# Kernel optimization log

Hardware: AMD Instinct MI355X
Metric: run time of the kernel (lower is better)

The kernel has to match this reference:

```python
import math
import jax, jax.numpy as jnp
import numpy as np

HEADS = 8
SCALE_BASE = 512.0
GN_EPS = 1e-5


def _gammas(heads):
    # 1 - exp(linspace(log(1/32), log(1/512), heads))
    return 1.0 - np.exp(np.linspace(math.log(1.0 / 32.0), math.log(1.0 / 512.0), heads))


def _xpos(x, downscale):
    # x: (N, S, d), d even. Faithful to torchscale XPOS with scale_base=512.
    N, S, d = x.shape
    half = d // 2
    scale = (jnp.arange(0, d, 2, dtype=jnp.float32) + 0.4 * d) / (1.4 * d)        # (half,)
    pos = jnp.arange(S, dtype=jnp.float32)
    sc = scale[None, :] ** (pos / SCALE_BASE)[:, None]                             # (S, half)
    inv_freq = 1.0 / (10000.0 ** (jnp.arange(half, dtype=jnp.float32) / half))
    sinusoid = pos[:, None] * inv_freq[None, :]                                    # (S, half)
    sin, cos = jnp.sin(sinusoid), jnp.cos(sinusoid)
    if downscale:
        sc = 1.0 / sc
    # duplicate_interleave == repeat each column twice adjacently
    sin_s = jnp.repeat(sin * sc, 2, axis=-1)                                       # (S, d)
    cos_s = jnp.repeat(cos * sc, 2, axis=-1)
    x1, x2 = x[..., ::2], x[..., 1::2]
    rot = jnp.stack((-x2, x1), axis=-1).reshape(x.shape)                           # rotate_every_two
    return x * cos_s + rot * sin_s


def setup_inputs() -> dict:
    key = jax.random.key(0)
    ks = jax.random.split(key, 6)
    B, S, H = 2, 2048, 1024
    h = HEADS
    d = H // h
    X = jax.random.normal(ks[0], (B, S, H), dtype=jnp.float32)
    # per-head projections, torch init: randn(d, d) / d
    W_Q = jax.random.normal(ks[1], (h, d, d), dtype=jnp.float32) / d
    W_K = jax.random.normal(ks[2], (h, d, d), dtype=jnp.float32) / d
    W_V = jax.random.normal(ks[3], (h, d, d), dtype=jnp.float32) / d
    W_G = jax.random.normal(ks[4], (H, H), dtype=jnp.float32) / H
    W_O = jax.random.normal(ks[5], (H, H), dtype=jnp.float32) / H
    gn_weight = jnp.ones((H,), dtype=jnp.float32)
    gn_bias = jnp.zeros((H,), dtype=jnp.float32)
    return {"X": X, "W_Q": W_Q, "W_K": W_K, "W_V": W_V,
            "W_G": W_G, "W_O": W_O, "gn_weight": gn_weight, "gn_bias": gn_bias}


def reference(X, W_Q, W_K, W_V, W_G, W_O, gn_weight, gn_bias):
    B, S, H = X.shape
    h = HEADS
    d = H // h
    gammas = jnp.asarray(_gammas(h), dtype=X.dtype)                                # (h,)

    Xh = X.reshape(B, S, h, d)
    Q = jnp.einsum('bshd,hde->bhse', Xh, W_Q)                                      # (B,h,S,d)
    K = jnp.einsum('bshd,hde->bhse', Xh, W_K)
    V = jnp.einsum('bshd,hde->bhse', Xh, W_V)

    Q = _xpos(Q.reshape(B * h, S, d), downscale=False).reshape(B, h, S, d)
    K = _xpos(K.reshape(B * h, S, d), downscale=True).reshape(B, h, S, d)

    # decay mask D[h, n, m] = gamma_h^(n-m) for n >= m else 0 (NaN-safe)
    n = jnp.arange(S)
    diff = n[:, None] - n[None, :]                                                 # (S,S)
    causal = (diff >= 0)
    D = (gammas[:, None, None] ** jnp.where(causal, diff, 0).astype(X.dtype)) \
        * causal[None].astype(X.dtype)                                             # (h,S,S)

    att = jnp.einsum('bhsd,bhtd->bhst', Q, K) * D[None]                            # (B,h,S,S)
    Y = jnp.einsum('bhst,bhtd->bshd', att, V).reshape(B, S, H)

    # GroupNorm(heads, hidden) over flattened (B*S, H), biased variance
    Yg = Y.reshape(B * S, h, d)
    mu = Yg.mean(axis=-1, keepdims=True)
    var = Yg.var(axis=-1, keepdims=True)
    Yn = ((Yg - mu) / jnp.sqrt(var + GN_EPS)).reshape(B * S, H)
    Yn = (Yn * gn_weight + gn_bias).reshape(B, S, H)

    G = X @ W_G
    return (G * jax.nn.sigmoid(G) * Yn) @ W_O
```

## Files before the change

### kernel.cpp

```cpp
#include <hip/hip_runtime.h>
#include <math.h>

#define NB 2
#define SEQ 2048
#define HD 1024
#define NH 8
#define DH 128
#define HALF 64

typedef __bf16 bf16_t;
typedef __attribute__((ext_vector_type(8))) __bf16 bf16x8;
typedef __attribute__((ext_vector_type(4))) __bf16 bf16x4;
typedef __attribute__((ext_vector_type(4))) float f32x4;

typedef __attribute__((address_space(1))) void gvoid;
typedef __attribute__((address_space(3))) void lvoid;

__device__ __forceinline__ void gld16(const bf16_t* g, bf16_t* l) {
  __builtin_amdgcn_global_load_lds((gvoid*)g, (lvoid*)l, 16, 0, 0);
}

__device__ __forceinline__ float head_l2g(int hh) {
  double ga = log(1.0/32.0), gbb = log(1.0/512.0);
  float gamma = (float)(1.0 - exp(ga + (double)hh * (gbb - ga) / 7.0));
  return log2f(gamma);
}

__global__ __launch_bounds__(256) void k_tables(float* __restrict__ tabs) {
  int idx = blockIdx.x * 256 + threadIdx.x;
  if (idx >= SEQ * HALF) return;
  int s = idx >> 6, i = idx & 63;
  float dd = (float)DH;
  float scale = (2.0f * (float)i + 0.4f * dd) / (1.4f * dd);
  float sc = expf(logf(scale) * ((float)s / 512.0f));
  float inv_freq = expf(-logf(10000.0f) * ((float)i / (float)HALF));
  float ang = (float)s * inv_freq;
  float sn, cs;
  sincosf(ang, &sn, &cs);
  float rsc = 1.0f / sc;
  tabs[idx]               = sn * sc;
  tabs[SEQ*HALF + idx]    = cs * sc;
  tabs[2*SEQ*HALF + idx]  = sn * rsc;
  tabs[3*SEQ*HALF + idx]  = cs * rsc;
}

__global__ __launch_bounds__(256) void k_wsplit(
    const float* __restrict__ in, bf16_t* __restrict__ oh, int M, int N) {
  __shared__ float tile[64][65];
  int z = blockIdx.z;
  in += (size_t)z * M * N; oh += (size_t)z * M * N;
  int r0 = blockIdx.y * 64, c0 = blockIdx.x * 64;
  int t = threadIdx.x;
  for (int idx = t; idx < 1024; idx += 256) {
    int r = idx >> 4, c4 = (idx & 15) * 4;
    float4 v = *(const float4*)(in + (size_t)(r0 + r) * N + c0 + c4);
    *(float4*)&tile[r][c4] = v;
  }
  __syncthreads();
  for (int idx = t; idx < 1024; idx += 256) {
    int c = idx >> 4, r4 = (idx & 15) * 4;
    bf16x4 h;
    #pragma unroll
    for (int j = 0; j < 4; ++j)
      h[j] = (bf16_t)tile[r4 + j][c];
    *(bf16x4*)(oh + (size_t)(c0 + c) * M + r0 + r4) = h;
  }
}

__global__ __launch_bounds__(256, 2) void k_qkv(
    const float* __restrict__ X, const float* __restrict__ tabs,
    const bf16_t* __restrict__ Wqt, const bf16_t* __restrict__ Wkt,
    const bf16_t* __restrict__ Wvt,
    bf16_t* __restrict__ Qo, bf16_t* __restrict__ Ko,
    bf16_t* __restrict__ VTo, bf16_t* __restrict__ Xhg) {
  __shared__ bf16_t Wsh[128][128];
  int t = threadIdx.x;
  int lane = t & 63, w = t >> 6;
  int lr = lane & 15, lg = lane >> 4;
  int s0 = blockIdx.x * 64;
  int hh = blockIdx.y;
  int b  = blockIdx.z;
  size_t bh = (size_t)(b*NH + hh);

  bf16x8 xh[4];
  {
    const float* xp = X + ((size_t)(b*SEQ + s0 + 16*w + lr)) * HD + hh*DH + 8*lg;
    #pragma unroll
    for (int ks = 0; ks < 4; ++ks) {
      float4 u = *(const float4*)(xp + 32*ks);
      float4 v = *(const float4*)(xp + 32*ks + 4);
      float fv[8] = {u.x,u.y,u.z,u.w,v.x,v.y,v.z,v.w};
      #pragma unroll
      for (int j = 0; j < 8; ++j) xh[ks][j] = (bf16_t)fv[j];
    }
  }
  {
    bf16_t* xo = Xhg + ((size_t)(b*SEQ + s0 + 16*w + lr)) * HD + hh*DH + 8*lg;
    #pragma unroll
    for (int ks = 0; ks < 4; ++ks)
      *(bf16x8*)(xo + 32*ks) = xh[ks];
  }

  const bf16_t* Wp[3] = {Wqt, Wkt, Wvt};

  for (int which = 0; which < 3; ++which) {
    const bf16_t* wp = Wp[which] + (size_t)hh * (DH*DH);
    __syncthreads();
    for (int idx = t; idx < 2048; idx += 256) {
      int e = idx >> 4, kb = idx & 15;
      int kbs = kb ^ (e & 7);
      *(bf16x8*)&Wsh[e][kbs*8] = *(const bf16x8*)(wp + (size_t)e*DH + kb*8);
    }
    __syncthreads();
    f32x4 yacc[8];
    #pragma unroll
    for (int i = 0; i < 8; ++i) yacc[i] = (f32x4){0.f,0.f,0.f,0.f};
    #pragma unroll
    for (int sub = 0; sub < 8; ++sub) {
      int e = 16*sub + lr;
      #pragma unroll
      for (int ks = 0; ks < 4; ++ks) {
        int ch = (lg + 4*ks) ^ (lr & 7);
        bf16x8 bhv = *(const bf16x8*)&Wsh[e][ch*8];
        yacc[sub] = __builtin_amdgcn_mfma_f32_16x16x32_bf16(xh[ks], bhv, yacc[sub], 0, 0, 0);
      }
    }
    if (which < 2) {
      const float* st = tabs + (which ? 2*SEQ*HALF : 0);
      const float* ct = st + SEQ*HALF;
      bf16_t* Op = which ? Ko : Qo;
      #pragma unroll
      for (int sub = 0; sub < 8; ++sub) {
        int e = 16*sub + lr;
        int i = e >> 1;
        #pragma unroll
        for (int reg = 0; reg < 4; ++reg) {
          float v = yacc[sub][reg];
          float p = __shfl_xor(v, 1);
          int srow = s0 + 16*w + 4*lg + reg;
          float sv = st[srow*HALF + i], cv = ct[srow*HALF + i];
          float o = v * cv + ((e & 1) ? p : -p) * sv;
          Op[(bh*SEQ + srow) * DH + e] = (bf16_t)o;
        }
      }
    } else {
      #pragma unroll
      for (int sub = 0; sub < 8; ++sub) {
        int e = 16*sub + lr;
        bf16x4 hv;
        #pragma unroll
        for (int reg = 0; reg < 4; ++reg)
          hv[reg] = (bf16_t)yacc[sub][reg];
        *(bf16x4*)(VTo + bh * (size_t)(DH*SEQ) + (size_t)e*SEQ + (s0 + 16*w + 4*lg)) = hv;
      }
    }
  }
}

__global__ __launch_bounds__(256, 1) void k_delta(
    const bf16_t* __restrict__ Kg, const bf16_t* __restrict__ VTg,
    bf16_t* __restrict__ DSt) {
  __shared__ bf16_t KT[128][128];
  __shared__ bf16_t Vd[128][128];
  int t = threadIdx.x;
  int lane = t & 63, w = t >> 6;
  int lr = lane & 15, lg = lane >> 4;
  int c = blockIdx.x, bh = blockIdx.y, hh = bh & 7;
  float l2g = head_l2g(hh);
  size_t kbase = (size_t)bh * SEQ * DH + (size_t)c * 128 * DH;
  size_t vtb   = (size_t)bh * DH * SEQ + (size_t)c * 128;

  for (int idx = t; idx < 2048; idx += 256) {
    int dc = idx >> 7, tau = idx & 127;
    bf16x8 h8 = *(const bf16x8*)(Kg + kbase + (size_t)tau*DH + dc*8);
    #pragma unroll
    for (int j = 0; j < 8; ++j) {
      int d = dc*8 + j;
      int col = (((tau>>3) ^ (d & 7)) << 3) | (tau & 7);
      KT[d][col] = h8[j];
    }
  }
  for (int idx = t; idx < 2048; idx += 256) {
    int dv = idx >> 4, tc = idx & 15;
    bf16x8 h8 = *(const bf16x8*)(VTg + vtb + (size_t)dv*SEQ + tc*8);
    bf16x8 oh;
    #pragma unroll
    for (int j = 0; j < 8; ++j) {
      int tau = tc*8 + j;
      oh[j] = (bf16_t)((float)h8[j] * exp2f(l2g * (float)(127 - tau)));
    }
    int cs = tc ^ (dv & 7);
    *(bf16x8*)&Vd[dv][cs*8] = oh;
  }
  __syncthreads();

  f32x4 acc[2][8];
  #pragma unroll
  for (int i = 0; i < 2; ++i)
    #pragma unroll
    for (int s = 0; s < 8; ++s) acc[i][s] = (f32x4){0.f,0.f,0.f,0.f};

  #pragma unroll
  for (int i = 0; i < 2; ++i) {
    int dv = 32*w + 16*i + lr;
    #pragma unroll
    for (int ks = 0; ks < 4; ++ks) {
      int ca = (lg + 4*ks) ^ (dv & 7);
      bf16x8 avh = *(const bf16x8*)&Vd[dv][ca*8];
      #pragma unroll
      for (int sub = 0; sub < 8; ++sub) {
        int dk = 16*sub + lr;
        int cb = (lg + 4*ks) ^ (dk & 7);
        bf16x8 bkh = *(const bf16x8*)&KT[dk][cb*8];
        acc[i][sub] = __builtin_amdgcn_mfma_f32_16x16x32_bf16(avh, bkh, acc[i][sub], 0, 0, 0);
      }
    }
  }
  size_t obase = ((size_t)bh * 16 + c) * 16384;
  #pragma unroll
  for (int i = 0; i < 2; ++i)
    #pragma unroll
    for (int sub = 0; sub < 8; ++sub)
      #pragma unroll
      for (int reg = 0; reg < 4; ++reg) {
        int dv = 32*w + 16*i + 4*lg + reg;
        int dk = 16*sub + lr;
        DSt[obase + (size_t)dv*128 + dk] = (bf16_t)acc[i][sub][reg];
      }
}

__global__ __launch_bounds__(256) void k_scan(bf16_t* __restrict__ DSt) {
  int t = threadIdx.x;
  int bh = blockIdx.y, hh = bh & 7;
  float l2g = head_l2g(hh);
  float g128 = exp2f(l2g * 128.0f);
  int dv = blockIdx.x * 16 + (t >> 4);
  int dk0 = (t & 15) * 8;
  size_t base = ((size_t)bh * 16) * 16384 + (size_t)dv*128 + dk0;
  float S[8] = {};
  for (int c = 0; c < 16; ++c) {
    size_t off = base + (size_t)c * 16384;
    bf16x8 dh = *(const bf16x8*)(DSt + off);
    bf16x8 sh;
    #pragma unroll
    for (int j = 0; j < 8; ++j) sh[j] = (bf16_t)S[j];
    *(bf16x8*)(DSt + off) = sh;
    #pragma unroll
    for (int j = 0; j < 8; ++j)
      S[j] = g128*S[j] + (float)dh[j];
  }
}

__global__ __launch_bounds__(512, 1) void k_ret(
    const bf16_t* __restrict__ Qg, const bf16_t* __restrict__ Kg,
    const bf16_t* __restrict__ VTg, const bf16_t* __restrict__ DSt,
    const float* __restrict__ gw, const float* __restrict__ gb,
    float* __restrict__ Yn) {
  __shared__ bf16_t Ksh[64][128];
  __shared__ bf16_t Vsh[128][64];
  __shared__ bf16_t Ph[128][64];
  int t = threadIdx.x;
  int lane = t & 63, w = t >> 6;
  int lr = lane & 15, lg = lane >> 4;
  int c = blockIdx.x, bh = blockIdx.y, hh = bh & 7;
  int s0 = c * 128;
  size_t base  = (size_t)bh * SEQ * DH;
  size_t vbase = (size_t)bh * DH * SEQ;
  float l2g = head_l2g(hh);
  float colf = exp2f(-l2g * (float)lr);
  float g16v[4];
  #pragma unroll
  for (int ts = 0; ts < 4; ++ts) g16v[ts] = exp2f(-l2g * (float)(16*ts));

  bf16x8 qh[4];
  {
    const bf16_t* qp = Qg + base + (size_t)(s0 + 16*w + lr) * DH + lg * 8;
    #pragma unroll
    for (int ks = 0; ks < 4; ++ks)
      qh[ks] = *(const bf16x8*)(qp + 32*ks);
  }
  f32x4 yacc[8];
  #pragma unroll
  for (int i = 0; i < 8; ++i) yacc[i] = (f32x4){0.f,0.f,0.f,0.f};

  for (int idx = t; idx < 1024; idx += 512) {
    int r = idx >> 4, kb = idx & 15;
    int kbs = kb ^ (r & 7);
    *(bf16x8*)&Ksh[r][kbs*8] = *(const bf16x8*)(Kg + base + (size_t)(s0 + r)*DH + kb*8);
  }
  for (int idx = t; idx < 1024; idx += 512) {
    int d = idx >> 3, cb = idx & 7;
    int cbs = cb ^ (d & 7);
    *(bf16x8*)&Vsh[d][cbs*8] = *(const bf16x8*)(VTg + vbase + (size_t)d*SEQ + s0 + cb*8);
  }

  {
    const bf16_t* sth = DSt + ((size_t)bh * 16 + c) * 16384;
    #pragma unroll
    for (int sub = 0; sub < 8; ++sub) {
      size_t ro = (size_t)(16*sub + lr) * 128 + 8*lg;
      #pragma unroll
      for (int ks = 0; ks < 4; ++ks) {
        bf16x8 bh_ = *(const bf16x8*)(sth + ro + 32*ks);
        yacc[sub] = __builtin_amdgcn_mfma_f32_16x16x32_bf16(qh[ks], bh_, yacc[sub], 0, 0, 0);
      }
    }
    float rowc[4];
    #pragma unroll
    for (int reg = 0; reg < 4; ++reg)
      rowc[reg] = exp2f(l2g * (float)(16*w + 4*lg + reg + 1));
    #pragma unroll
    for (int sub = 0; sub < 8; ++sub)
      #pragma unroll
      for (int reg = 0; reg < 4; ++reg)
        yacc[sub][reg] *= rowc[reg];
  }
  __syncthreads();

  for (int kt = 0; kt < 2; ++kt) {
    int t0 = kt * 64;
    if (kt == 1) {
      __syncthreads();
      for (int idx = t; idx < 1024; idx += 512) {
        int r = idx >> 4, kb = idx & 15;
        int kbs = kb ^ (r & 7);
        *(bf16x8*)&Ksh[r][kbs*8] = *(const bf16x8*)(Kg + base + (size_t)(s0 + 64 + r)*DH + kb*8);
      }
      for (int idx = t; idx < 1024; idx += 512) {
        int d = idx >> 3, cb = idx & 7;
        int cbs = cb ^ (d & 7);
        *(bf16x8*)&Vsh[d][cbs*8] = *(const bf16x8*)(VTg + vbase + (size_t)d*SEQ + s0 + 64 + cb*8);
      }
    }
    __syncthreads();
    if (!(kt == 1 && w < 4)) {
      float rowf[4];
      #pragma unroll
      for (int reg = 0; reg < 4; ++reg)
        rowf[reg] = exp2f(l2g * (float)(16*w + 4*lg + reg - t0));

      #pragma unroll
      for (int ts = 0; ts < 4; ++ts) {
        f32x4 sacc = (f32x4){0.f,0.f,0.f,0.f};
        int trow = 16*ts + lr;
        #pragma unroll
        for (int ks = 0; ks < 4; ++ks) {
          int kbs = (4*ks + lg) ^ (trow & 7);
          bf16x8 kh8 = *(const bf16x8*)&Ksh[trow][kbs*8];
          sacc = __builtin_amdgcn_mfma_f32_16x16x32_bf16(qh[ks], kh8, sacc, 0, 0, 0);
        }
        float cf = colf * g16v[ts];
        #pragma unroll
        for (int reg = 0; reg < 4; ++reg) {
          int qloc = 4*lg + reg;
          int diff = (16*w + qloc) - (t0 + trow);
          float p = (diff >= 0) ? sacc[reg] * (rowf[reg] * cf) : 0.0f;
          int cb = (trow >> 3) ^ (qloc & 7);
          Ph[16*w + qloc][cb*8 + (trow & 7)] = (bf16_t)p;
        }
      }
      #pragma unroll
      for (int ks = 0; ks < 2; ++ks) {
        int prow = 16*w + lr;
        int pcb = (4*ks + lg) ^ (lr & 7);
        bf16x8 pah = *(const bf16x8*)&Ph[prow][pcb*8];
        #pragma unroll
        for (int sub = 0; sub < 8; ++sub) {
          int drow = 16*sub + lr;
          int vcb = (4*ks + lg) ^ (drow & 7);
          bf16x8 vh8 = *(const bf16x8*)&Vsh[drow][vcb*8];
          yacc[sub] = __builtin_amdgcn_mfma_f32_16x16x32_bf16(pah, vh8, yacc[sub], 0, 0, 0);
        }
      }
    }
  }

  float s1v[4] = {0.f,0.f,0.f,0.f}, s2v[4] = {0.f,0.f,0.f,0.f};
  #pragma unroll
  for (int sub = 0; sub < 8; ++sub)
    #pragma unroll
    for (int reg = 0; reg < 4; ++reg) {
      float v = yacc[sub][reg];
      s1v[reg] += v;
      s2v[reg] += v * v;
    }
  #pragma unroll
  for (int off = 8; off; off >>= 1)
    #pragma unroll
    for (int reg = 0; reg < 4; ++reg) {
      s1v[reg] += __shfl_xor(s1v[reg], off);
      s2v[reg] += __shfl_xor(s2v[reg], off);
    }
  float gwv[8], gbv[8];
  #pragma unroll
  for (int sub = 0; sub < 8; ++sub) {
    gwv[sub] = gw[hh*DH + 16*sub + lr];
    gbv[sub] = gb[hh*DH + 16*sub + lr];
  }
  int b = bh >> 3;
  #pragma unroll
  for (int reg = 0; reg < 4; ++reg) {
    float mean = s1v[reg] * (1.0f/128.0f);
    float var = s2v[reg] * (1.0f/128.0f) - mean*mean;
    float inv = rsqrtf(var + 1e-5f);
    int srow = s0 + 16*w + 4*lg + reg;
    float* op = Yn + (size_t)(b*SEQ + srow) * HD + hh*DH;
    #pragma unroll
    for (int sub = 0; sub < 8; ++sub)
      op[16*sub + lr] = (yacc[sub][reg] - mean) * inv * gwv[sub] + gbv[sub];
  }
}

__global__ __launch_bounds__(512, 1) void k_gemm(
    const bf16_t* __restrict__ Ag, const bf16_t* __restrict__ Bg,
    const float* __restrict__ E,
    bf16_t* __restrict__ Oh, float* __restrict__ Of, int mode) {
  __shared__ bf16_t SB[2][2][128][64];
  int t = threadIdx.x;
  int lane = t & 63, w = t >> 6;
  int lr = lane & 15, lg = lane >> 4;
  int wr = w >> 1, wc = w & 1;
  int bid = blockIdx.x;
  int swz = (bid & 7) * 32 + (bid >> 3);
  int n0 = (swz & 7) * 128, m0 = (swz >> 3) * 128;

  const bf16_t* srcs[2] = { Ag + (size_t)m0 * HD, Bg + (size_t)n0 * HD };

  f32x4 acc[2][4];
  #pragma unroll
  for (int i = 0; i < 2; ++i)
    #pragma unroll
    for (int j = 0; j < 4; ++j) acc[i][j] = (f32x4){0.f,0.f,0.f,0.f};

  int srow = lane >> 3, sch = lane & 7;

  #pragma unroll
  for (int bi = 0; bi < 2; ++bi)
    #pragma unroll
    for (int i = 0; i < 2; ++i) {
      int row = w*16 + i*8 + srow;
      int kc = (sch ^ (row & 7)) * 8;
      gld16(srcs[bi] + (size_t)row*HD + kc, &SB[bi][0][w*16 + i*8][0]);
    }
  __syncthreads();

  int buf = 0;
  for (int kt = 0; kt < 16; ++kt) {
    if (kt + 1 < 16) {
      int k0 = (kt + 1) * 64;
      #pragma unroll
      for (int bi = 0; bi < 2; ++bi)
        #pragma unroll
        for (int i = 0; i < 2; ++i) {
          int row = w*16 + i*8 + srow;
          int kc = (sch ^ (row & 7)) * 8;
          gld16(srcs[bi] + (size_t)row*HD + k0 + kc, &SB[bi][buf^1][w*16 + i*8][0]);
        }
    }
    #pragma unroll
    for (int ks = 0; ks < 2; ++ks) {
      bf16x8 a_[2], b_[4];
      #pragma unroll
      for (int mf = 0; mf < 2; ++mf) {
        int row = wr*32 + mf*16 + lr;
        int ch = (lg + 4*ks) ^ (row & 7);
        a_[mf] = *(const bf16x8*)&SB[0][buf][row][ch*8];
      }
      #pragma unroll
      for (int nf = 0; nf < 4; ++nf) {
        int row = wc*64 + nf*16 + lr;
        int ch = (lg + 4*ks) ^ (row & 7);
        b_[nf] = *(const bf16x8*)&SB[1][buf][row][ch*8];
      }
      #pragma unroll
      for (int mf = 0; mf < 2; ++mf)
        #pragma unroll
        for (int nf = 0; nf < 4; ++nf)
          acc[mf][nf] = __builtin_amdgcn_mfma_f32_16x16x32_bf16(a_[mf], b_[nf], acc[mf][nf], 0, 0, 0);
    }
    __syncthreads();
    buf ^= 1;
  }
  #pragma unroll
  for (int mf = 0; mf < 2; ++mf) {
    #pragma unroll
    for (int nf = 0; nf < 4; ++nf) {
      #pragma unroll
      for (int reg = 0; reg < 4; ++reg) {
        int m = m0 + wr*32 + mf*16 + 4*lg + reg;
        int n = n0 + wc*64 + nf*16 + lr;
        float g = acc[mf][nf][reg];
        size_t off = (size_t)m * HD + n;
        if (mode == 1) {
          float sg = 1.0f / (1.0f + expf(-g));
          Oh[off] = (bf16_t)(g * sg * E[off]);
        } else {
          Of[off] = g;
        }
      }
    }
  }
}

extern "C" void kernel_launch(void* const* d_in, const int* in_sizes, int n_in,
                              void* d_out, int out_size, void* d_ws, size_t ws_size,
                              hipStream_t stream) {
  const float* X  = (const float*)d_in[0];
  const float* Wq = (const float*)d_in[1];
  const float* Wk = (const float*)d_in[2];
  const float* Wv = (const float*)d_in[3];
  const float* Wg = (const float*)d_in[4];
  const float* Wo = (const float*)d_in[5];
  const float* gw = (const float*)d_in[6];
  const float* gb = (const float*)d_in[7];
  float* out = (float*)d_out;
  float* ws = (float*)d_ws;

  float* tabs = ws;
  bf16_t* Q   = (bf16_t*)(ws + 524288);
  bf16_t* K   = Q + 4194304;
  bf16_t* VT  = K + 4194304;
  float*  Yn  = (float*)(VT + 4194304);
  bf16_t* DSt = (bf16_t*)(Yn + 4194304);
  bf16_t* Wqt = DSt + 4194304;
  bf16_t* Wkt = Wqt + 131072;
  bf16_t* Wvt = Wkt + 131072;
  bf16_t* Wgt = Wvt + 131072;
  bf16_t* Wot = Wgt + 1048576;
  bf16_t* Xh  = Wot + 1048576;
  bf16_t* A2  = Q;

  k_tables<<<dim3(512), dim3(256), 0, stream>>>(tabs);
  k_wsplit<<<dim3(2, 2, 8), dim3(256), 0, stream>>>(Wq, Wqt, DH, DH);
  k_wsplit<<<dim3(2, 2, 8), dim3(256), 0, stream>>>(Wk, Wkt, DH, DH);
  k_wsplit<<<dim3(2, 2, 8), dim3(256), 0, stream>>>(Wv, Wvt, DH, DH);
  k_wsplit<<<dim3(16, 16, 1), dim3(256), 0, stream>>>(Wg, Wgt, HD, HD);
  k_wsplit<<<dim3(16, 16, 1), dim3(256), 0, stream>>>(Wo, Wot, HD, HD);
  k_qkv<<<dim3(32, 8, 2), dim3(256), 0, stream>>>(X, tabs, Wqt, Wkt, Wvt,
                                                  Q, K, VT, Xh);
  k_delta<<<dim3(16, 16), dim3(256), 0, stream>>>(K, VT, DSt);
  k_scan<<<dim3(8, 16), dim3(256), 0, stream>>>(DSt);
  k_ret<<<dim3(16, 16), dim3(512), 0, stream>>>(Q, K, VT, DSt, gw, gb, Yn);
  k_gemm<<<dim3(256), dim3(512), 0, stream>>>(Xh, Wgt, Yn, A2, nullptr, 1);
  k_gemm<<<dim3(256), dim3(512), 0, stream>>>(A2, Wot, nullptr, nullptr, out, 0);
}
```

Before: 116.4 us.

## Merge prep kernels, store normalized output in bf16, retile gated GEMMs

Merges the table-generation kernel and the five weight transpose/convert launches into a single prep kernel that dispatches on block index, removing five launches. The group-norm output Yn is now written in bf16 instead of fp32, which halves its write and re-read traffic in the gating GEMM. The two final GEMMs switch from 128x128 tiles with 512 threads to 64x128 tiles with 256 threads and two blocks per CU, doubling the grid and using an XCD-aware block mapping. Storing Yn in bf16 adds rounding error, and the smaller tiles reuse each loaded B tile across fewer rows.

```diff
diff --git a/kernel.cpp b/kernel.cpp
--- a/kernel.cpp
+++ b/kernel.cpp
@@ -26,30 +26,11 @@
   return log2f(gamma);
 }
 
-__global__ __launch_bounds__(256) void k_tables(float* __restrict__ tabs) {
-  int idx = blockIdx.x * 256 + threadIdx.x;
-  if (idx >= SEQ * HALF) return;
-  int s = idx >> 6, i = idx & 63;
-  float dd = (float)DH;
-  float scale = (2.0f * (float)i + 0.4f * dd) / (1.4f * dd);
-  float sc = expf(logf(scale) * ((float)s / 512.0f));
-  float inv_freq = expf(-logf(10000.0f) * ((float)i / (float)HALF));
-  float ang = (float)s * inv_freq;
-  float sn, cs;
-  sincosf(ang, &sn, &cs);
-  float rsc = 1.0f / sc;
-  tabs[idx]               = sn * sc;
-  tabs[SEQ*HALF + idx]    = cs * sc;
-  tabs[2*SEQ*HALF + idx]  = sn * rsc;
-  tabs[3*SEQ*HALF + idx]  = cs * rsc;
-}
-
-__global__ __launch_bounds__(256) void k_wsplit(
-    const float* __restrict__ in, bf16_t* __restrict__ oh, int M, int N) {
-  __shared__ float tile[64][65];
-  int z = blockIdx.z;
+__device__ void wsplit_body(const float* __restrict__ in, bf16_t* __restrict__ oh,
+                            int M, int N, int bx, int by, int z,
+                            float (*tile)[65]) {
   in += (size_t)z * M * N; oh += (size_t)z * M * N;
-  int r0 = blockIdx.y * 64, c0 = blockIdx.x * 64;
+  int r0 = by * 64, c0 = bx * 64;
   int t = threadIdx.x;
   for (int idx = t; idx < 1024; idx += 256) {
     int r = idx >> 4, c4 = (idx & 15) * 4;
@@ -64,6 +45,46 @@
     for (int j = 0; j < 4; ++j)
       h[j] = (bf16_t)tile[r4 + j][c];
     *(bf16x4*)(oh + (size_t)(c0 + c) * M + r0 + r4) = h;
+  }
+}
+
+__global__ __launch_bounds__(256) void k_prep(
+    const float* __restrict__ Wq, const float* __restrict__ Wk,
+    const float* __restrict__ Wv, const float* __restrict__ Wg,
+    const float* __restrict__ Wo,
+    float* __restrict__ tabs, bf16_t* __restrict__ Wqt,
+    bf16_t* __restrict__ Wkt, bf16_t* __restrict__ Wvt,
+    bf16_t* __restrict__ Wgt, bf16_t* __restrict__ Wot) {
+  __shared__ float tile[64][65];
+  int b = blockIdx.x;
+  if (b < 512) {
+    int idx = b * 256 + threadIdx.x;
+    int s = idx >> 6, i = idx & 63;
+    float dd = (float)DH;
+    float scale = (2.0f * (float)i + 0.4f * dd) / (1.4f * dd);
+    float sc = expf(logf(scale) * ((float)s / 512.0f));
+    float inv_freq = expf(-logf(10000.0f) * ((float)i / (float)HALF));
+    float ang = (float)s * inv_freq;
+    float sn, cs;
+    sincosf(ang, &sn, &cs);
+    float rsc = 1.0f / sc;
+    tabs[idx]               = sn * sc;
+    tabs[SEQ*HALF + idx]    = cs * sc;
+    tabs[2*SEQ*HALF + idx]  = sn * rsc;
+    tabs[3*SEQ*HALF + idx]  = cs * rsc;
+  } else if (b < 608) {
+    int i = b - 512;
+    int which = i >> 5;
+    int j = i & 31;
+    const float* in = (which == 0) ? Wq : (which == 1) ? Wk : Wv;
+    bf16_t* oh = (which == 0) ? Wqt : (which == 1) ? Wkt : Wvt;
+    wsplit_body(in, oh, DH, DH, j & 1, (j >> 1) & 1, j >> 2, tile);
+  } else {
+    int i = b - 608;
+    int which = i >> 8;
+    int j = i & 255;
+    wsplit_body(which ? Wo : Wg, which ? Wot : Wgt, HD, HD,
+                j & 15, j >> 4, 0, tile);
   }
 }
 
@@ -255,7 +276,7 @@
     const bf16_t* __restrict__ Qg, const bf16_t* __restrict__ Kg,
     const bf16_t* __restrict__ VTg, const bf16_t* __restrict__ DSt,
     const float* __restrict__ gw, const float* __restrict__ gb,
-    float* __restrict__ Yn) {
+    bf16_t* __restrict__ Yn) {
   __shared__ bf16_t Ksh[64][128];
   __shared__ bf16_t Vsh[128][64];
   __shared__ bf16_t Ph[128][64];
@@ -404,27 +425,31 @@
     float var = s2v[reg] * (1.0f/128.0f) - mean*mean;
     float inv = rsqrtf(var + 1e-5f);
     int srow = s0 + 16*w + 4*lg + reg;
-    float* op = Yn + (size_t)(b*SEQ + srow) * HD + hh*DH;
+    bf16_t* op = Yn + (size_t)(b*SEQ + srow) * HD + hh*DH;
     #pragma unroll
     for (int sub = 0; sub < 8; ++sub)
-      op[16*sub + lr] = (yacc[sub][reg] - mean) * inv * gwv[sub] + gbv[sub];
-  }
-}
-
-__global__ __launch_bounds__(512, 1) void k_gemm(
+      op[16*sub + lr] = (bf16_t)((yacc[sub][reg] - mean) * inv * gwv[sub] + gbv[sub]);
+  }
+}
+
+__global__ __launch_bounds__(256, 2) void k_gemm(
     const bf16_t* __restrict__ Ag, const bf16_t* __restrict__ Bg,
-    const float* __restrict__ E,
+    const bf16_t* __restrict__ E,
     bf16_t* __restrict__ Oh, float* __restrict__ Of, int mode) {
-  __shared__ bf16_t SB[2][2][128][64];
+  __shared__ bf16_t SA[2][64][64];
+  __shared__ bf16_t SBB[2][128][64];
   int t = threadIdx.x;
   int lane = t & 63, w = t >> 6;
   int lr = lane & 15, lg = lane >> 4;
   int wr = w >> 1, wc = w & 1;
   int bid = blockIdx.x;
-  int swz = (bid & 7) * 32 + (bid >> 3);
-  int n0 = (swz & 7) * 128, m0 = (swz >> 3) * 128;
-
-  const bf16_t* srcs[2] = { Ag + (size_t)m0 * HD, Bg + (size_t)n0 * HD };
+  int xcd = bid & 7, local = bid >> 3;
+  int mp = xcd * 8 + (local >> 3);
+  int np = local & 7;
+  int m0 = mp * 64, n0 = np * 128;
+
+  const bf16_t* As = Ag + (size_t)m0 * HD;
+  const bf16_t* Bs = Bg + (size_t)n0 * HD;
 
   f32x4 acc[2][4];
   #pragma unroll
@@ -434,14 +459,20 @@
 
   int srow = lane >> 3, sch = lane & 7;
 
-  #pragma unroll
-  for (int bi = 0; bi < 2; ++bi)
+  {
     #pragma unroll
     for (int i = 0; i < 2; ++i) {
       int row = w*16 + i*8 + srow;
       int kc = (sch ^ (row & 7)) * 8;
-      gld16(srcs[bi] + (size_t)row*HD + kc, &SB[bi][0][w*16 + i*8][0]);
-    }
+      gld16(As + (size_t)row*HD + kc, &SA[0][w*16 + i*8][0]);
+    }
+    #pragma unroll
+    for (int i = 0; i < 4; ++i) {
+      int row = w*32 + i*8 + srow;
+      int kc = (sch ^ (row & 7)) * 8;
+      gld16(Bs + (size_t)row*HD + kc, &SBB[0][w*32 + i*8][0]);
+    }
+  }
   __syncthreads();
 
   int buf = 0;
@@ -449,13 +480,17 @@
     if (kt + 1 < 16) {
       int k0 = (kt + 1) * 64;
       #pragma unroll
-      for (int bi = 0; bi < 2; ++bi)
-        #pragma unroll
-        for (int i = 0; i < 2; ++i) {
-          int row = w*16 + i*8 + srow;
-          int kc = (sch ^ (row & 7)) * 8;
-          gld16(srcs[bi] + (size_t)row*HD + k0 + kc, &SB[bi][buf^1][w*16 + i*8][0]);
-        }
+      for (int i = 0; i < 2; ++i) {
+        int row = w*16 + i*8 + srow;
+        int kc = (sch ^ (row & 7)) * 8;
+        gld16(As + (size_t)row*HD + k0 + kc, &SA[buf^1][w*16 + i*8][0]);
+      }
+      #pragma unroll
+      for (int i = 0; i < 4; ++i) {
+        int row = w*32 + i*8 + srow;
+        int kc = (sch ^ (row & 7)) * 8;
+        gld16(Bs + (size_t)row*HD + k0 + kc, &SBB[buf^1][w*32 + i*8][0]);
+      }
     }
     #pragma unroll
     for (int ks = 0; ks < 2; ++ks) {
@@ -464,13 +499,13 @@
       for (int mf = 0; mf < 2; ++mf) {
         int row = wr*32 + mf*16 + lr;
         int ch = (lg + 4*ks) ^ (row & 7);
-        a_[mf] = *(const bf16x8*)&SB[0][buf][row][ch*8];
+        a_[mf] = *(const bf16x8*)&SA[buf][row][ch*8];
       }
       #pragma unroll
       for (int nf = 0; nf < 4; ++nf) {
         int row = wc*64 + nf*16 + lr;
         int ch = (lg + 4*ks) ^ (row & 7);
-        b_[nf] = *(const bf16x8*)&SB[1][buf][row][ch*8];
+        b_[nf] = *(const bf16x8*)&SBB[buf][row][ch*8];
       }
       #pragma unroll
       for (int mf = 0; mf < 2; ++mf)
@@ -493,7 +528,7 @@
         size_t off = (size_t)m * HD + n;
         if (mode == 1) {
           float sg = 1.0f / (1.0f + expf(-g));
-          Oh[off] = (bf16_t)(g * sg * E[off]);
+          Oh[off] = (bf16_t)(g * sg * (float)E[off]);
         } else {
           Of[off] = g;
         }
@@ -520,8 +555,8 @@
   bf16_t* Q   = (bf16_t*)(ws + 524288);
   bf16_t* K   = Q + 4194304;
   bf16_t* VT  = K + 4194304;
-  float*  Yn  = (float*)(VT + 4194304);
-  bf16_t* DSt = (bf16_t*)(Yn + 4194304);
+  bf16_t* Yn  = VT + 4194304;
+  bf16_t* DSt = Yn + 4194304;
   bf16_t* Wqt = DSt + 4194304;
   bf16_t* Wkt = Wqt + 131072;
   bf16_t* Wvt = Wkt + 131072;
@@ -530,17 +565,13 @@
   bf16_t* Xh  = Wot + 1048576;
   bf16_t* A2  = Q;
 
-  k_tables<<<dim3(512), dim3(256), 0, stream>>>(tabs);
-  k_wsplit<<<dim3(2, 2, 8), dim3(256), 0, stream>>>(Wq, Wqt, DH, DH);
-  k_wsplit<<<dim3(2, 2, 8), dim3(256), 0, stream>>>(Wk, Wkt, DH, DH);
-  k_wsplit<<<dim3(2, 2, 8), dim3(256), 0, stream>>>(Wv, Wvt, DH, DH);
-  k_wsplit<<<dim3(16, 16, 1), dim3(256), 0, stream>>>(Wg, Wgt, HD, HD);
-  k_wsplit<<<dim3(16, 16, 1), dim3(256), 0, stream>>>(Wo, Wot, HD, HD);
+  k_prep<<<dim3(1120), dim3(256), 0, stream>>>(Wq, Wk, Wv, Wg, Wo, tabs,
+                                               Wqt, Wkt, Wvt, Wgt, Wot);
   k_qkv<<<dim3(32, 8, 2), dim3(256), 0, stream>>>(X, tabs, Wqt, Wkt, Wvt,
                                                   Q, K, VT, Xh);
   k_delta<<<dim3(16, 16), dim3(256), 0, stream>>>(K, VT, DSt);
   k_scan<<<dim3(8, 16), dim3(256), 0, stream>>>(DSt);
   k_ret<<<dim3(16, 16), dim3(512), 0, stream>>>(Q, K, VT, DSt, gw, gb, Yn);
-  k_gemm<<<dim3(256), dim3(512), 0, stream>>>(Xh, Wgt, Yn, A2, nullptr, 1);
-  k_gemm<<<dim3(256), dim3(512), 0, stream>>>(A2, Wot, nullptr, nullptr, out, 0);
-}
+  k_gemm<<<dim3(512), dim3(256), 0, stream>>>(Xh, Wgt, Yn, A2, nullptr, 1);
+  k_gemm<<<dim3(512), dim3(256), 0, stream>>>(A2, Wot, nullptr, nullptr, out, 0);
+}
```

After: 108.0 us. -7.2%, faster.
